# Performance work log

Measured on AMD Instinct MI355X. Metric: run time of the kernel, lower is better.

## Reference

```python
import jax, jax.numpy as jnp
import numpy as np

CONF_THR = 0.3   # cfg.THRESHOLD_PREDICT_CONF
NMS_THR = 0.5    # cfg.THRESHOLD_PREDICT_NMS
TOP_K = 2048     # fixed candidate budget (padded NMS, replaces boolean-mask gather)


def _build_grids():
    # YOLOv3 @ 608: feature maps 19/38/76, 3 anchors each -> HWA = 22743
    fsizes = [19, 38, 76]
    anchors_px = [
        [(116, 90), (156, 198), (373, 326)],
        [(30, 61), (62, 45), (59, 119)],
        [(10, 13), (16, 30), (33, 23)],
    ]
    img = 608.0
    gs, ans, ifs = [], [], []
    for fs, ancs in zip(fsizes, anchors_px):
        ys, xs = np.meshgrid(np.arange(fs), np.arange(fs), indexing='ij')
        cell = np.stack([xs, ys], -1).reshape(-1, 1, 2).astype(np.float32)
        cell = np.broadcast_to(cell, (fs * fs, 3, 2)).reshape(-1, 2)
        a = np.asarray(ancs, np.float32) / img
        a = np.broadcast_to(a[None], (fs * fs, 3, 2)).reshape(-1, 2)
        gs.append(cell)
        ans.append(np.ascontiguousarray(a))
        ifs.append(np.full((fs * fs * 3, 1), 1.0 / fs, np.float32))
    return (np.concatenate(gs), np.concatenate(ans), np.concatenate(ifs))


def setup_inputs() -> dict:
    key = jax.random.key(0)
    k1, k2, k3 = jax.random.split(key, 3)
    B, HWA, C = 32, 22743, 80
    grid_xy, anchor_wh, inv_fsize = _build_grids()
    return {
        'pconf': jax.random.normal(k1, (B, HWA, 1), jnp.float32),
        'pcls': jax.random.normal(k2, (B, HWA, C), jnp.float32),
        'ptxywh': jax.random.normal(k3, (B, HWA, 4), jnp.float32),
        'grid_xy': jnp.asarray(grid_xy),
        'anchor_wh': jnp.asarray(anchor_wh),
        'inv_fsize': jnp.asarray(inv_fsize),
    }


def _decode_ltrb(ptxywh, grid_xy, anchor_wh, inv_fsize):
    # boxes_decode4yolo3: cxcy = (sigmoid(txy)+grid)/fsize ; wh = exp(twh)*anchor
    cxcy = (jax.nn.sigmoid(ptxywh[..., :2]) + grid_xy) * inv_fsize
    wh = jnp.exp(ptxywh[..., 2:4]) * anchor_wh
    half = 0.5 * wh
    return jnp.concatenate([cxcy - half, cxcy + half], axis=-1)


def _iou_one_to_many(box, boxes):
    lt = jnp.maximum(box[:2], boxes[:, :2])
    rb = jnp.minimum(box[2:], boxes[:, 2:])
    wh = jnp.clip(rb - lt, 0.0)
    inter = wh[:, 0] * wh[:, 1]
    a1 = (box[2] - box[0]) * (box[3] - box[1])
    a2 = (boxes[:, 2] - boxes[:, 0]) * (boxes[:, 3] - boxes[:, 1])
    return inter / (a1 + a2 - inter + 1e-9)


def reference(pconf, pcls, ptxywh, grid_xy, anchor_wh, inv_fsize):
    B, HWA, C = pcls.shape
    conf = jax.nn.sigmoid(pconf[..., 0])                 # [B,HWA]
    cls_s = jax.nn.sigmoid(pcls)
    cls_conf = cls_s.max(-1)                             # [B,HWA]
    plabels = jnp.argmax(cls_s, -1).astype(jnp.int32) + 1  # labels +1 as original
    scores = cls_conf * conf                             # [B,HWA]
    pltrb = jnp.clip(_decode_ltrb(ptxywh, grid_xy, anchor_wh, inv_fsize), 0.0, 1.0)

    # threshold mask -> fixed top-K candidates (padded replacement for boolean gather)
    flat_scores = scores.reshape(-1)
    masked = jnp.where(flat_scores > CONF_THR, flat_scores, -1.0)
    top_s, top_i = jax.lax.top_k(masked, TOP_K)          # descending order
    valid = top_s > CONF_THR
    ids_b = (top_i // HWA).astype(jnp.int32)
    boxes = pltrb.reshape(-1, 4)[top_i]                  # [K,4]
    labels = plabels.reshape(-1)[top_i]                  # [K]
    scr = flat_scores[top_i]                             # [K]

    # per-(image,label) NMS via coordinate offset trick (label_nms equivalent)
    off = (ids_b.astype(jnp.float32) * (C + 2) + labels.astype(jnp.float32)) * 4.0
    boxes_off = boxes + off[:, None]
    idx = jnp.arange(TOP_K)

    def body(i, keep):
        iou = _iou_one_to_many(boxes_off[i], boxes_off)
        supp = keep[i] & (iou > NMS_THR) & (idx > i)
        return keep & ~supp

    keep = jax.lax.fori_loop(0, TOP_K, body, valid)
    scores_out = jnp.where(keep, scr, 0.0)
    boxes_out = jnp.where(keep[:, None], boxes, 0.0)
    return ids_b, boxes_out, labels, scores_out, keep
```

## Files before the change

### kernel.cpp

```cpp
#include <hip/hip_runtime.h>
#include <math.h>

#define HWA   22743
#define NBATCH 32
#define NROW  (HWA * NBATCH)
#define NC    80
#define TOPK  2048
#define CAND_CAP 4096
#define CONF_THR 0.3f
#define NMS_THR  0.5f
#define NBIN  4096
#define BIN0  0xBE999u
#define NZCAP 224

__device__ __forceinline__ unsigned int ford(float f) {
    unsigned int u = __float_as_uint(f);
    return (u & 0x80000000u) ? ~u : (u | 0x80000000u);
}
__device__ __forceinline__ float fdec(unsigned int o) {
    unsigned int u = (o & 0x80000000u) ? (o & 0x7fffffffu) : ~o;
    return __uint_as_float(u);
}
__device__ __forceinline__ float sigmoidf(float x) {
    return 1.0f / (1.0f + expf(-x));
}

__global__ void k_zero(unsigned int* __restrict__ z, int nwords) {
    int t = blockIdx.x * 1024 + threadIdx.x;
    if (t < nwords) z[t] = 0u;
}

__global__ void k_score(const float* __restrict__ pconf, const float* __restrict__ pcls,
                        unsigned int* __restrict__ skey, int* __restrict__ labels,
                        unsigned int* __restrict__ hist) {
    int gtid = blockIdx.x * blockDim.x + threadIdx.x;
    int wave = gtid >> 6;
    int lane = threadIdx.x & 63;
    int sub  = lane >> 4;
    int sl   = lane & 15;
    int nwaves = (gridDim.x * blockDim.x) >> 6;
    for (int base = wave * 4; base < NROW; base += nwaves * 4) {
        int i = base + sub;
        const float* row = pcls + (size_t)i * NC;
        float4 q = *(const float4*)(row + 4 * sl);
        float  e = row[64 + sl];
        float v0 = q.x; int i0 = 4 * sl;
        if (q.y > v0) { v0 = q.y; i0 = 4 * sl + 1; }
        if (q.z > v0) { v0 = q.z; i0 = 4 * sl + 2; }
        if (q.w > v0) { v0 = q.w; i0 = 4 * sl + 3; }
        if (e  > v0) { v0 = e;   i0 = 64 + sl; }
        #pragma unroll
        for (int off = 8; off > 0; off >>= 1) {
            float ov = __shfl_xor(v0, off, 64);
            int   oi = __shfl_xor(i0, off, 64);
            if (ov > v0 || (ov == v0 && oi < i0)) { v0 = ov; i0 = oi; }
        }
        if (sl == 0) {
            float cls_conf = sigmoidf(v0);
            float conf     = sigmoidf(pconf[i]);
            float score    = cls_conf * conf;
            float masked   = (score > CONF_THR) ? score : -1.0f;
            unsigned int o = ford(masked);
            skey[i]   = o;
            labels[i] = i0 + 1;
            if (score > CONF_THR) atomicAdd(&hist[(o >> 12) - BIN0], 1u);
        }
    }
}

__global__ __launch_bounds__(1024) void k_findT(const unsigned int* __restrict__ hist,
                                                unsigned int* __restrict__ scal) {
    __shared__ unsigned int a[1024];
    int tid = threadIdx.x;
    unsigned int r0 = hist[4095 - 4 * tid];
    unsigned int r1 = hist[4094 - 4 * tid];
    unsigned int r2 = hist[4093 - 4 * tid];
    unsigned int r3 = hist[4092 - 4 * tid];
    unsigned int local = r0 + r1 + r2 + r3;
    a[tid] = local;
    __syncthreads();
    for (int off = 1; off < 1024; off <<= 1) {
        unsigned int v = a[tid];
        unsigned int ad = (tid >= off) ? a[tid - off] : 0u;
        __syncthreads();
        a[tid] = v + ad;
        __syncthreads();
    }
    unsigned int inc = a[tid];
    unsigned int pre = inc - local;
    unsigned int total = a[1023];
    if (tid == 0 && total < TOPK) scal[0] = BIN0;
    if (pre < TOPK && inc >= TOPK) {
        unsigned int c = pre;
        unsigned int rr[4] = {r0, r1, r2, r3};
        #pragma unroll
        for (int j = 0; j < 4; ++j) {
            unsigned int nc = c + rr[j];
            if (c < TOPK && nc >= TOPK) {
                int p = 4 * tid + j;
                scal[0] = BIN0 + (unsigned int)(4095 - p);
            }
            c = nc;
        }
    }
}

__global__ void k_compact(const unsigned int* __restrict__ skey,
                          unsigned long long* __restrict__ cand,
                          unsigned int* __restrict__ scal) {
    unsigned int T = scal[0];
    int lane = threadIdx.x & 63;
    int stride = gridDim.x * blockDim.x;
    for (int i = blockIdx.x * blockDim.x + threadIdx.x; i < NROW; i += stride) {
        unsigned int o = skey[i];
        bool take = (o >> 12) >= T;
        unsigned long long m = __ballot(take);
        if (m) {
            int leader = __ffsll(m) - 1;
            unsigned int bse = 0;
            if (lane == leader) bse = atomicAdd(&scal[1], (unsigned int)__popcll(m));
            bse = __shfl(bse, leader, 64);
            if (take) {
                unsigned int pos = bse + (unsigned int)__popcll(m & ((1ull << lane) - 1ull));
                if (pos < CAND_CAP)
                    cand[pos] = ((unsigned long long)o << 32) | (unsigned int)(~(unsigned int)i);
            }
        }
    }
}

__global__ __launch_bounds__(256) void k_rank(const unsigned long long* __restrict__ cand,
                                              const unsigned int* __restrict__ scal,
                                              unsigned int* __restrict__ rankbuf) {
    __shared__ unsigned long long tile[256];
    unsigned int M = scal[1]; if (M > CAND_CAP) M = CAND_CAP;
    int ct = blockIdx.x >> 4;
    int st = blockIdx.x & 15;
    int c  = ct * 256 + threadIdx.x;
    int jb = st * 256;
    tile[threadIdx.x] = (jb + threadIdx.x < (int)M) ? cand[jb + threadIdx.x] : 0ull;
    __syncthreads();
    if (c < (int)M) {
        unsigned long long myk = cand[c];
        int lim = (int)M - jb; if (lim > 256) lim = 256;
        int r = 0;
        #pragma unroll 8
        for (int j = 0; j < lim; ++j) r += (tile[j] > myk) ? 1 : 0;
        if (r) atomicAdd(&rankbuf[c], (unsigned int)r);
    }
}

__global__ __launch_bounds__(256) void k_scatprep(const unsigned long long* __restrict__ cand,
                          const unsigned int* __restrict__ rankbuf,
                          const unsigned int* __restrict__ scal,
                          const int* __restrict__ labels,
                          const float* __restrict__ ptxywh,
                          const float* __restrict__ grid_xy,
                          const float* __restrict__ anchor_wh,
                          const float* __restrict__ inv_fsize,
                          unsigned int* __restrict__ bidx_a, unsigned int* __restrict__ label_a,
                          float* __restrict__ score_a, float4* __restrict__ box_a,
                          float4* __restrict__ boxoff_a, unsigned long long* __restrict__ keepmask) {
    unsigned int M = scal[1]; if (M > CAND_CAP) M = CAND_CAP;
    int t = blockIdx.x * 256 + threadIdx.x;
    if (t < (int)M) {
        unsigned int rk = rankbuf[t];
        if (rk < TOPK) {
            unsigned long long key = cand[t];
            unsigned int idx = ~(unsigned int)(key & 0xffffffffull);
            unsigned int o = (unsigned int)(key >> 32);
            float score = fdec(o);
            unsigned int b = idx / HWA;
            unsigned int r = idx - b * HWA;
            int lab = labels[idx];
            const float* tp = ptxywh + (size_t)idx * 4;
            float tx = tp[0], ty = tp[1], tw = tp[2], th = tp[3];
            float gx = grid_xy[2 * r], gy = grid_xy[2 * r + 1];
            float aw = anchor_wh[2 * r], ah = anchor_wh[2 * r + 1];
            float invf = inv_fsize[r];
            float cx = (sigmoidf(tx) + gx) * invf;
            float cy = (sigmoidf(ty) + gy) * invf;
            float w = expf(tw) * aw;
            float h = expf(th) * ah;
            float hx = 0.5f * w, hy = 0.5f * h;
            float l = cx - hx, tt = cy - hy, rr = cx + hx, bb = cy + hy;
            l  = fminf(fmaxf(l, 0.0f), 1.0f);
            tt = fminf(fmaxf(tt, 0.0f), 1.0f);
            rr = fminf(fmaxf(rr, 0.0f), 1.0f);
            bb = fminf(fmaxf(bb, 0.0f), 1.0f);
            float off = ((float)b * (float)(NC + 2) + (float)lab) * 4.0f;
            float4 bx; bx.x = l; bx.y = tt; bx.z = rr; bx.w = bb;
            float4 bo; bo.x = l + off; bo.y = tt + off; bo.z = rr + off; bo.w = bb + off;
            box_a[rk] = bx;
            boxoff_a[rk] = bo;
            bidx_a[rk] = b;
            label_a[rk] = (unsigned int)lab;
            score_a[rk] = score;
            atomicOr(&keepmask[rk >> 6], 1ull << (rk & 63));
        }
    } else if (t < TOPK) {
        float4 z; z.x = 0.0f; z.y = 0.0f; z.z = 0.0f; z.w = 0.0f;
        box_a[t] = z; boxoff_a[t] = z;
        bidx_a[t] = 0u; label_a[t] = 0u; score_a[t] = 0.0f;
    }
}

__global__ void k_supp(const float4* __restrict__ boxoff,
                       unsigned long long* __restrict__ supp,
                       unsigned long long* __restrict__ rownz) {
    __shared__ unsigned long long anyw;
    int i = blockIdx.x;
    if (threadIdx.x == 0) anyw = 0ull;
    __syncthreads();
    float4 bi = boxoff[i];
    float a1 = (bi.z - bi.x) * (bi.w - bi.y);
    unsigned long long myany = 0ull;
    for (int jt = 0; jt < 8; ++jt) {
        int j = jt * 256 + threadIdx.x;
        float4 bj = boxoff[j];
        float ltx = fmaxf(bi.x, bj.x), lty = fmaxf(bi.y, bj.y);
        float rbx = fminf(bi.z, bj.z), rby = fminf(bi.w, bj.w);
        float wx = rbx - ltx; if (wx < 0.0f) wx = 0.0f;
        float wy = rby - lty; if (wy < 0.0f) wy = 0.0f;
        float inter = wx * wy;
        float a2 = (bj.z - bj.x) * (bj.w - bj.y);
        float iou = inter / (a1 + a2 - inter + 1e-9f);
        unsigned long long m = __ballot(iou > NMS_THR);
        int w = jt * 4 + (threadIdx.x >> 6);
        if ((threadIdx.x & 63) == 0) supp[(size_t)i * 32 + w] = m;
        unsigned long long masked;
        int base = w * 64;
        if (base + 63 <= i) masked = 0ull;
        else if (base > i) masked = m;
        else {
            int d = i - base;
            unsigned long long le = (d == 63) ? ~0ull : ((1ull << (d + 1)) - 1ull);
            masked = m & ~le;
        }
        if ((threadIdx.x & 63) == 0) myany |= masked;
    }
    if ((threadIdx.x & 63) == 0 && myany) atomicOr(&anyw, myany);
    __syncthreads();
    if (threadIdx.x == 0 && anyw) atomicOr(&rownz[i >> 6], 1ull << (i & 63));
}

__global__ __launch_bounds__(256) void k_scanout(const unsigned long long* __restrict__ supp,
                        const unsigned long long* __restrict__ rownz,
                        const unsigned long long* __restrict__ keepmask,
                        const unsigned int* __restrict__ bidx_a,
                        const unsigned int* __restrict__ label_a,
                        const float* __restrict__ score_a,
                        const float4* __restrict__ box_a,
                        float* __restrict__ out) {
    __shared__ unsigned long long kw[32];
    __shared__ unsigned long long rz[32];
    __shared__ unsigned int base[33];
    __shared__ unsigned short rowid[NZCAP];
    __shared__ unsigned long long sm[NZCAP][32];
    int tid = threadIdx.x;
    if (tid < 32) { kw[tid] = keepmask[tid]; rz[tid] = rownz[tid]; }
    __syncthreads();
    if (tid == 0) {
        unsigned int acc = 0;
        for (int w = 0; w < 32; ++w) { base[w] = acc; acc += (unsigned int)__popcll(rz[w]); }
        base[32] = acc;
    }
    __syncthreads();
    unsigned int A = base[32];
    unsigned int Acap = (A < NZCAP) ? A : NZCAP;
    if (tid < 32) {
        unsigned long long m = rz[tid];
        unsigned int p = base[tid];
        while (m) {
            int b = __ffsll(m) - 1;
            if (p < NZCAP) rowid[p] = (unsigned short)(tid * 64 + b);
            ++p;
            m &= m - 1ull;
        }
    }
    __syncthreads();
    for (unsigned int p0 = 0; p0 < Acap; p0 += 8) {
        unsigned int p = p0 + (unsigned int)(tid >> 5);
        if (p < Acap) {
            int i = rowid[p];
            sm[p][tid & 31] = supp[(size_t)i * 32 + (tid & 31)];
        }
    }
    __syncthreads();
    for (int wi = 0; wi < 32; ++wi) {
        unsigned long long processed = 0ull;
        while (true) {
            unsigned long long act = kw[wi] & rz[wi] & ~processed;
            if (!act) break;
            int b = __ffsll(act) - 1;
            int i = wi * 64 + b;
            unsigned int p = base[wi] +
                (unsigned int)__popcll(rz[wi] & ((1ull << b) - 1ull));
            if (tid < 32) {
                unsigned long long rw = (p < NZCAP) ? sm[p][tid]
                                                    : supp[(size_t)i * 32 + tid];
                if (tid < wi) rw = 0ull;
                else if (tid == wi) {
                    unsigned long long le = (b == 63) ? ~0ull : ((1ull << (b + 1)) - 1ull);
                    rw &= ~le;
                }
                kw[tid] &= ~rw;
            }
            __syncthreads();
            processed |= (1ull << b);
        }
    }
    __syncthreads();
    for (int k = tid; k < TOPK; k += 256) {
        bool kp = (kw[k >> 6] >> (k & 63)) & 1ull;
        float4 bx = box_a[k];
        out[k] = (float)bidx_a[k];
        float* ob = out + TOPK + 4 * k;
        ob[0] = kp ? bx.x : 0.0f;
        ob[1] = kp ? bx.y : 0.0f;
        ob[2] = kp ? bx.z : 0.0f;
        ob[3] = kp ? bx.w : 0.0f;
        out[TOPK * 5 + k] = (float)label_a[k];
        out[TOPK * 6 + k] = kp ? score_a[k] : 0.0f;
        out[TOPK * 7 + k] = kp ? 1.0f : 0.0f;
    }
}

extern "C" void kernel_launch(void* const* d_in, const int* in_sizes, int n_in,
                              void* d_out, int out_size, void* d_ws, size_t ws_size,
                              hipStream_t stream) {
    const float* pconf     = (const float*)d_in[0];
    const float* pcls      = (const float*)d_in[1];
    const float* ptxywh    = (const float*)d_in[2];
    const float* grid_xy   = (const float*)d_in[3];
    const float* anchor_wh = (const float*)d_in[4];
    const float* inv_fsize = (const float*)d_in[5];
    float* out = (float*)d_out;

    char* ws = (char*)d_ws;
    const size_t O_HIST   = 0;
    const size_t O_SCAL   = O_HIST + NBIN * 4;
    const size_t O_ROWNZ  = O_SCAL + 64;
    const size_t O_KEEPM  = O_ROWNZ + 256;
    const size_t O_RANK   = O_KEEPM + 256;
    const size_t O_ZEND   = O_RANK + (size_t)CAND_CAP * 4;
    const int    ZERO_WORDS = (int)(O_ZEND / 4);
    const size_t O_CAND   = O_ZEND;
    const size_t O_SKEY   = O_CAND + (size_t)CAND_CAP * 8;
    const size_t O_LABELS = O_SKEY + (size_t)NROW * 4;
    const size_t O_BIDX   = O_LABELS + (size_t)NROW * 4;
    const size_t O_LAB2   = O_BIDX + (size_t)TOPK * 4;
    const size_t O_SCORE  = O_LAB2 + (size_t)TOPK * 4;
    const size_t O_BOX    = O_SCORE + (size_t)TOPK * 4;
    const size_t O_BOXOFF = O_BOX + (size_t)TOPK * 16;
    const size_t O_SUPP   = O_BOXOFF + (size_t)TOPK * 16;

    unsigned int* hist  = (unsigned int*)(ws + O_HIST);
    unsigned int* scal  = (unsigned int*)(ws + O_SCAL);
    unsigned long long* rownz = (unsigned long long*)(ws + O_ROWNZ);
    unsigned long long* keepm = (unsigned long long*)(ws + O_KEEPM);
    unsigned int* rankbuf = (unsigned int*)(ws + O_RANK);
    unsigned long long* cand   = (unsigned long long*)(ws + O_CAND);
    unsigned int* skey  = (unsigned int*)(ws + O_SKEY);
    int*          labels = (int*)(ws + O_LABELS);
    unsigned int* bidx_a  = (unsigned int*)(ws + O_BIDX);
    unsigned int* label_a = (unsigned int*)(ws + O_LAB2);
    float*        score_a = (float*)(ws + O_SCORE);
    float4*       box_a   = (float4*)(ws + O_BOX);
    float4*       boxoff_a = (float4*)(ws + O_BOXOFF);
    unsigned long long* supp = (unsigned long long*)(ws + O_SUPP);

    k_zero<<<9, 1024, 0, stream>>>((unsigned int*)ws, ZERO_WORDS);
    k_score<<<2048, 256, 0, stream>>>(pconf, pcls, skey, labels, hist);
    k_findT<<<1, 1024, 0, stream>>>(hist, scal);
    k_compact<<<1024, 256, 0, stream>>>(skey, cand, scal);
    k_rank<<<256, 256, 0, stream>>>(cand, scal, rankbuf);
    k_scatprep<<<CAND_CAP / 256, 256, 0, stream>>>(cand, rankbuf, scal, labels, ptxywh,
                                                   grid_xy, anchor_wh, inv_fsize,
                                                   bidx_a, label_a, score_a,
                                                   box_a, boxoff_a, keepm);
    k_supp<<<TOPK, 256, 0, stream>>>(boxoff_a, supp, rownz);
    k_scanout<<<1, 256, 0, stream>>>(supp, rownz, keepm, bidx_a, label_a, score_a,
                                     box_a, out);
}
```

Before: 168.4 us.

## Fuse post-score pipeline into one cooperative kernel with grid syncs

Replaces six separate launches (threshold search, compaction, ranking, scatter/decode, suppression matrix, scan/output) with a single cooperative kernel of 256 blocks. Grid-wide syncs separate the stages, and every block recomputes the threshold from the histogram itself. The suppression stage now stages all offset boxes in shared memory and each block handles 8 rows. This targets launch overhead and inter-kernel gaps in a latency-bound tail, at the cost of grid-sync overhead, reduced parallelism in the compaction and suppression stages, and a larger shared-memory footprint.

```diff
diff --git a/kernel.cpp b/kernel.cpp
--- a/kernel.cpp
+++ b/kernel.cpp
@@ -1,5 +1,8 @@
 #include <hip/hip_runtime.h>
+#include <hip/hip_cooperative_groups.h>
 #include <math.h>
+
+namespace cg = cooperative_groups;
 
 #define HWA   22743
 #define NBATCH 32
@@ -12,6 +15,23 @@
 #define NBIN  4096
 #define BIN0  0xBE999u
 #define NZCAP 224
+
+#define O_HIST   ((size_t)0)
+#define O_SCAL   (O_HIST + (size_t)NBIN * 4)
+#define O_ROWNZ  (O_SCAL + 64)
+#define O_KEEPM  (O_ROWNZ + 256)
+#define O_RANK   (O_KEEPM + 256)
+#define O_ZEND   (O_RANK + (size_t)CAND_CAP * 4)
+#define ZERO_WORDS ((int)(O_ZEND / 4))
+#define O_CAND   O_ZEND
+#define O_SKEY   (O_CAND + (size_t)CAND_CAP * 8)
+#define O_LABELS (O_SKEY + (size_t)NROW * 4)
+#define O_BIDX   (O_LABELS + (size_t)NROW * 4)
+#define O_LAB2   (O_BIDX + (size_t)TOPK * 4)
+#define O_SCORE  (O_LAB2 + (size_t)TOPK * 4)
+#define O_BOX    (O_SCORE + (size_t)TOPK * 4)
+#define O_BOXOFF (O_BOX + (size_t)TOPK * 16)
+#define O_SUPP   (O_BOXOFF + (size_t)TOPK * 16)
 
 __device__ __forceinline__ unsigned int ford(float f) {
     unsigned int u = __float_as_uint(f);
@@ -68,261 +88,273 @@
     }
 }
 
-__global__ __launch_bounds__(1024) void k_findT(const unsigned int* __restrict__ hist,
-                                                unsigned int* __restrict__ scal) {
-    __shared__ unsigned int a[1024];
+__global__ __launch_bounds__(256, 1) void k_tail(char* __restrict__ ws,
+        const float* __restrict__ ptxywh, const float* __restrict__ grid_xy,
+        const float* __restrict__ anchor_wh, const float* __restrict__ inv_fsize,
+        float* __restrict__ out) {
+    unsigned int* hist  = (unsigned int*)(ws + O_HIST);
+    unsigned int* scal  = (unsigned int*)(ws + O_SCAL);
+    unsigned long long* rownz = (unsigned long long*)(ws + O_ROWNZ);
+    unsigned long long* keepm = (unsigned long long*)(ws + O_KEEPM);
+    unsigned int* rankbuf = (unsigned int*)(ws + O_RANK);
+    unsigned long long* cand = (unsigned long long*)(ws + O_CAND);
+    unsigned int* skey  = (unsigned int*)(ws + O_SKEY);
+    const int* labels   = (const int*)(ws + O_LABELS);
+    unsigned int* bidx_a  = (unsigned int*)(ws + O_BIDX);
+    unsigned int* label_a = (unsigned int*)(ws + O_LAB2);
+    float*        score_a = (float*)(ws + O_SCORE);
+    float4*       box_a   = (float4*)(ws + O_BOX);
+    float4*       boxoff_a = (float4*)(ws + O_BOXOFF);
+    unsigned long long* supp = (unsigned long long*)(ws + O_SUPP);
+
+    cg::grid_group gg = cg::this_grid();
     int tid = threadIdx.x;
-    unsigned int r0 = hist[4095 - 4 * tid];
-    unsigned int r1 = hist[4094 - 4 * tid];
-    unsigned int r2 = hist[4093 - 4 * tid];
-    unsigned int r3 = hist[4092 - 4 * tid];
-    unsigned int local = r0 + r1 + r2 + r3;
-    a[tid] = local;
-    __syncthreads();
-    for (int off = 1; off < 1024; off <<= 1) {
-        unsigned int v = a[tid];
-        unsigned int ad = (tid >= off) ? a[tid - off] : 0u;
-        __syncthreads();
-        a[tid] = v + ad;
-        __syncthreads();
-    }
-    unsigned int inc = a[tid];
-    unsigned int pre = inc - local;
-    unsigned int total = a[1023];
-    if (tid == 0 && total < TOPK) scal[0] = BIN0;
-    if (pre < TOPK && inc >= TOPK) {
-        unsigned int c = pre;
-        unsigned int rr[4] = {r0, r1, r2, r3};
-        #pragma unroll
-        for (int j = 0; j < 4; ++j) {
-            unsigned int nc = c + rr[j];
-            if (c < TOPK && nc >= TOPK) {
-                int p = 4 * tid + j;
-                scal[0] = BIN0 + (unsigned int)(4095 - p);
-            }
-            c = nc;
-        }
-    }
-}
-
-__global__ void k_compact(const unsigned int* __restrict__ skey,
-                          unsigned long long* __restrict__ cand,
-                          unsigned int* __restrict__ scal) {
-    unsigned int T = scal[0];
-    int lane = threadIdx.x & 63;
-    int stride = gridDim.x * blockDim.x;
-    for (int i = blockIdx.x * blockDim.x + threadIdx.x; i < NROW; i += stride) {
-        unsigned int o = skey[i];
-        bool take = (o >> 12) >= T;
-        unsigned long long m = __ballot(take);
-        if (m) {
-            int leader = __ffsll(m) - 1;
-            unsigned int bse = 0;
-            if (lane == leader) bse = atomicAdd(&scal[1], (unsigned int)__popcll(m));
-            bse = __shfl(bse, leader, 64);
-            if (take) {
-                unsigned int pos = bse + (unsigned int)__popcll(m & ((1ull << lane) - 1ull));
-                if (pos < CAND_CAP)
-                    cand[pos] = ((unsigned long long)o << 32) | (unsigned int)(~(unsigned int)i);
-            }
-        }
-    }
-}
-
-__global__ __launch_bounds__(256) void k_rank(const unsigned long long* __restrict__ cand,
-                                              const unsigned int* __restrict__ scal,
-                                              unsigned int* __restrict__ rankbuf) {
-    __shared__ unsigned long long tile[256];
-    unsigned int M = scal[1]; if (M > CAND_CAP) M = CAND_CAP;
-    int ct = blockIdx.x >> 4;
-    int st = blockIdx.x & 15;
-    int c  = ct * 256 + threadIdx.x;
-    int jb = st * 256;
-    tile[threadIdx.x] = (jb + threadIdx.x < (int)M) ? cand[jb + threadIdx.x] : 0ull;
-    __syncthreads();
-    if (c < (int)M) {
-        unsigned long long myk = cand[c];
-        int lim = (int)M - jb; if (lim > 256) lim = 256;
-        int r = 0;
-        #pragma unroll 8
-        for (int j = 0; j < lim; ++j) r += (tile[j] > myk) ? 1 : 0;
-        if (r) atomicAdd(&rankbuf[c], (unsigned int)r);
-    }
-}
-
-__global__ __launch_bounds__(256) void k_scatprep(const unsigned long long* __restrict__ cand,
-                          const unsigned int* __restrict__ rankbuf,
-                          const unsigned int* __restrict__ scal,
-                          const int* __restrict__ labels,
-                          const float* __restrict__ ptxywh,
-                          const float* __restrict__ grid_xy,
-                          const float* __restrict__ anchor_wh,
-                          const float* __restrict__ inv_fsize,
-                          unsigned int* __restrict__ bidx_a, unsigned int* __restrict__ label_a,
-                          float* __restrict__ score_a, float4* __restrict__ box_a,
-                          float4* __restrict__ boxoff_a, unsigned long long* __restrict__ keepmask) {
-    unsigned int M = scal[1]; if (M > CAND_CAP) M = CAND_CAP;
-    int t = blockIdx.x * 256 + threadIdx.x;
-    if (t < (int)M) {
-        unsigned int rk = rankbuf[t];
-        if (rk < TOPK) {
-            unsigned long long key = cand[t];
-            unsigned int idx = ~(unsigned int)(key & 0xffffffffull);
-            unsigned int o = (unsigned int)(key >> 32);
-            float score = fdec(o);
-            unsigned int b = idx / HWA;
-            unsigned int r = idx - b * HWA;
-            int lab = labels[idx];
-            const float* tp = ptxywh + (size_t)idx * 4;
-            float tx = tp[0], ty = tp[1], tw = tp[2], th = tp[3];
-            float gx = grid_xy[2 * r], gy = grid_xy[2 * r + 1];
-            float aw = anchor_wh[2 * r], ah = anchor_wh[2 * r + 1];
-            float invf = inv_fsize[r];
-            float cx = (sigmoidf(tx) + gx) * invf;
-            float cy = (sigmoidf(ty) + gy) * invf;
-            float w = expf(tw) * aw;
-            float h = expf(th) * ah;
-            float hx = 0.5f * w, hy = 0.5f * h;
-            float l = cx - hx, tt = cy - hy, rr = cx + hx, bb = cy + hy;
-            l  = fminf(fmaxf(l, 0.0f), 1.0f);
-            tt = fminf(fmaxf(tt, 0.0f), 1.0f);
-            rr = fminf(fmaxf(rr, 0.0f), 1.0f);
-            bb = fminf(fmaxf(bb, 0.0f), 1.0f);
-            float off = ((float)b * (float)(NC + 2) + (float)lab) * 4.0f;
-            float4 bx; bx.x = l; bx.y = tt; bx.z = rr; bx.w = bb;
-            float4 bo; bo.x = l + off; bo.y = tt + off; bo.z = rr + off; bo.w = bb + off;
-            box_a[rk] = bx;
-            boxoff_a[rk] = bo;
-            bidx_a[rk] = b;
-            label_a[rk] = (unsigned int)lab;
-            score_a[rk] = score;
-            atomicOr(&keepmask[rk >> 6], 1ull << (rk & 63));
-        }
-    } else if (t < TOPK) {
-        float4 z; z.x = 0.0f; z.y = 0.0f; z.z = 0.0f; z.w = 0.0f;
-        box_a[t] = z; boxoff_a[t] = z;
-        bidx_a[t] = 0u; label_a[t] = 0u; score_a[t] = 0.0f;
-    }
-}
-
-__global__ void k_supp(const float4* __restrict__ boxoff,
-                       unsigned long long* __restrict__ supp,
-                       unsigned long long* __restrict__ rownz) {
-    __shared__ unsigned long long anyw;
-    int i = blockIdx.x;
-    if (threadIdx.x == 0) anyw = 0ull;
-    __syncthreads();
-    float4 bi = boxoff[i];
-    float a1 = (bi.z - bi.x) * (bi.w - bi.y);
-    unsigned long long myany = 0ull;
-    for (int jt = 0; jt < 8; ++jt) {
-        int j = jt * 256 + threadIdx.x;
-        float4 bj = boxoff[j];
-        float ltx = fmaxf(bi.x, bj.x), lty = fmaxf(bi.y, bj.y);
-        float rbx = fminf(bi.z, bj.z), rby = fminf(bi.w, bj.w);
-        float wx = rbx - ltx; if (wx < 0.0f) wx = 0.0f;
-        float wy = rby - lty; if (wy < 0.0f) wy = 0.0f;
-        float inter = wx * wy;
-        float a2 = (bj.z - bj.x) * (bj.w - bj.y);
-        float iou = inter / (a1 + a2 - inter + 1e-9f);
-        unsigned long long m = __ballot(iou > NMS_THR);
-        int w = jt * 4 + (threadIdx.x >> 6);
-        if ((threadIdx.x & 63) == 0) supp[(size_t)i * 32 + w] = m;
-        unsigned long long masked;
-        int base = w * 64;
-        if (base + 63 <= i) masked = 0ull;
-        else if (base > i) masked = m;
-        else {
-            int d = i - base;
-            unsigned long long le = (d == 63) ? ~0ull : ((1ull << (d + 1)) - 1ull);
-            masked = m & ~le;
-        }
-        if ((threadIdx.x & 63) == 0) myany |= masked;
-    }
-    if ((threadIdx.x & 63) == 0 && myany) atomicOr(&anyw, myany);
-    __syncthreads();
-    if (threadIdx.x == 0 && anyw) atomicOr(&rownz[i >> 6], 1ull << (i & 63));
-}
-
-__global__ __launch_bounds__(256) void k_scanout(const unsigned long long* __restrict__ supp,
-                        const unsigned long long* __restrict__ rownz,
-                        const unsigned long long* __restrict__ keepmask,
-                        const unsigned int* __restrict__ bidx_a,
-                        const unsigned int* __restrict__ label_a,
-                        const float* __restrict__ score_a,
-                        const float4* __restrict__ box_a,
-                        float* __restrict__ out) {
+    int bid = blockIdx.x;
+
+    __shared__ unsigned long long sm[NZCAP][32];
     __shared__ unsigned long long kw[32];
     __shared__ unsigned long long rz[32];
-    __shared__ unsigned int base[33];
+    __shared__ unsigned int sbase[33];
     __shared__ unsigned short rowid[NZCAP];
-    __shared__ unsigned long long sm[NZCAP][32];
-    int tid = threadIdx.x;
-    if (tid < 32) { kw[tid] = keepmask[tid]; rz[tid] = rownz[tid]; }
-    __syncthreads();
-    if (tid == 0) {
-        unsigned int acc = 0;
-        for (int w = 0; w < 32; ++w) { base[w] = acc; acc += (unsigned int)__popcll(rz[w]); }
-        base[32] = acc;
-    }
-    __syncthreads();
-    unsigned int A = base[32];
-    unsigned int Acap = (A < NZCAP) ? A : NZCAP;
-    if (tid < 32) {
-        unsigned long long m = rz[tid];
-        unsigned int p = base[tid];
-        while (m) {
-            int b = __ffsll(m) - 1;
-            if (p < NZCAP) rowid[p] = (unsigned short)(tid * 64 + b);
-            ++p;
-            m &= m - 1ull;
-        }
-    }
-    __syncthreads();
-    for (unsigned int p0 = 0; p0 < Acap; p0 += 8) {
-        unsigned int p = p0 + (unsigned int)(tid >> 5);
-        if (p < Acap) {
-            int i = rowid[p];
-            sm[p][tid & 31] = supp[(size_t)i * 32 + (tid & 31)];
-        }
-    }
-    __syncthreads();
-    for (int wi = 0; wi < 32; ++wi) {
-        unsigned long long processed = 0ull;
-        while (true) {
-            unsigned long long act = kw[wi] & rz[wi] & ~processed;
-            if (!act) break;
-            int b = __ffsll(act) - 1;
-            int i = wi * 64 + b;
-            unsigned int p = base[wi] +
-                (unsigned int)__popcll(rz[wi] & ((1ull << b) - 1ull));
-            if (tid < 32) {
-                unsigned long long rw = (p < NZCAP) ? sm[p][tid]
-                                                    : supp[(size_t)i * 32 + tid];
-                if (tid < wi) rw = 0ull;
-                else if (tid == wi) {
-                    unsigned long long le = (b == 63) ? ~0ull : ((1ull << (b + 1)) - 1ull);
-                    rw &= ~le;
+    __shared__ unsigned int sT;
+    __shared__ unsigned long long anyw;
+
+    {
+        unsigned int* a = (unsigned int*)sm;
+        unsigned int r[16];
+        unsigned int local = 0;
+        #pragma unroll
+        for (int j = 0; j < 16; ++j) {
+            r[j] = hist[4095 - (tid * 16 + j)];
+            local += r[j];
+        }
+        a[tid] = local;
+        __syncthreads();
+        for (int off = 1; off < 256; off <<= 1) {
+            unsigned int v = a[tid];
+            unsigned int ad = (tid >= off) ? a[tid - off] : 0u;
+            __syncthreads();
+            a[tid] = v + ad;
+            __syncthreads();
+        }
+        unsigned int inc = a[tid];
+        unsigned int pre = inc - local;
+        unsigned int total = a[255];
+        if (tid == 0 && total < TOPK) sT = BIN0;
+        if (pre < TOPK && inc >= TOPK) {
+            unsigned int c = pre;
+            #pragma unroll
+            for (int j = 0; j < 16; ++j) {
+                unsigned int nc = c + r[j];
+                if (c < TOPK && nc >= TOPK) {
+                    int p = tid * 16 + j;
+                    sT = BIN0 + (unsigned int)(4095 - p);
                 }
-                kw[tid] &= ~rw;
-            }
-            __syncthreads();
-            processed |= (1ull << b);
-        }
-    }
-    __syncthreads();
-    for (int k = tid; k < TOPK; k += 256) {
-        bool kp = (kw[k >> 6] >> (k & 63)) & 1ull;
-        float4 bx = box_a[k];
-        out[k] = (float)bidx_a[k];
-        float* ob = out + TOPK + 4 * k;
-        ob[0] = kp ? bx.x : 0.0f;
-        ob[1] = kp ? bx.y : 0.0f;
-        ob[2] = kp ? bx.z : 0.0f;
-        ob[3] = kp ? bx.w : 0.0f;
-        out[TOPK * 5 + k] = (float)label_a[k];
-        out[TOPK * 6 + k] = kp ? score_a[k] : 0.0f;
-        out[TOPK * 7 + k] = kp ? 1.0f : 0.0f;
+                c = nc;
+            }
+        }
+        __syncthreads();
+    }
+    unsigned int T = sT;
+
+    {
+        int lane = tid & 63;
+        int stride = 256 * 256;
+        for (int i = bid * 256 + tid; i < NROW; i += stride) {
+            unsigned int o = skey[i];
+            bool take = (o >> 12) >= T;
+            unsigned long long m = __ballot(take);
+            if (m) {
+                int leader = __ffsll(m) - 1;
+                unsigned int bse = 0;
+                if (lane == leader) bse = atomicAdd(&scal[1], (unsigned int)__popcll(m));
+                bse = __shfl(bse, leader, 64);
+                if (take) {
+                    unsigned int pos = bse + (unsigned int)__popcll(m & ((1ull << lane) - 1ull));
+                    if (pos < CAND_CAP)
+                        cand[pos] = ((unsigned long long)o << 32) | (unsigned int)(~(unsigned int)i);
+                }
+            }
+        }
+    }
+    gg.sync();
+
+    {
+        unsigned long long* tile = (unsigned long long*)sm;
+        unsigned int M = scal[1]; if (M > CAND_CAP) M = CAND_CAP;
+        int ct = bid >> 4;
+        int st = bid & 15;
+        int c  = ct * 256 + tid;
+        int jb = st * 256;
+        tile[tid] = (jb + tid < (int)M) ? cand[jb + tid] : 0ull;
+        __syncthreads();
+        if (c < (int)M) {
+            unsigned long long myk = cand[c];
+            int lim = (int)M - jb; if (lim > 256) lim = 256;
+            int r = 0;
+            #pragma unroll 8
+            for (int j = 0; j < lim; ++j) r += (tile[j] > myk) ? 1 : 0;
+            if (r) atomicAdd(&rankbuf[c], (unsigned int)r);
+        }
+    }
+    gg.sync();
+
+    if (bid < CAND_CAP / 256) {
+        unsigned int M = scal[1]; if (M > CAND_CAP) M = CAND_CAP;
+        int t = bid * 256 + tid;
+        if (t < (int)M) {
+            unsigned int rk = rankbuf[t];
+            if (rk < TOPK) {
+                unsigned long long key = cand[t];
+                unsigned int idx = ~(unsigned int)(key & 0xffffffffull);
+                unsigned int o = (unsigned int)(key >> 32);
+                float score = fdec(o);
+                unsigned int b = idx / HWA;
+                unsigned int r = idx - b * HWA;
+                int lab = labels[idx];
+                const float* tp = ptxywh + (size_t)idx * 4;
+                float tx = tp[0], ty = tp[1], tw = tp[2], th = tp[3];
+                float gx = grid_xy[2 * r], gy = grid_xy[2 * r + 1];
+                float aw = anchor_wh[2 * r], ah = anchor_wh[2 * r + 1];
+                float invf = inv_fsize[r];
+                float cx = (sigmoidf(tx) + gx) * invf;
+                float cy = (sigmoidf(ty) + gy) * invf;
+                float w = expf(tw) * aw;
+                float h = expf(th) * ah;
+                float hx = 0.5f * w, hy = 0.5f * h;
+                float l = cx - hx, tt = cy - hy, rr = cx + hx, bb = cy + hy;
+                l  = fminf(fmaxf(l, 0.0f), 1.0f);
+                tt = fminf(fmaxf(tt, 0.0f), 1.0f);
+                rr = fminf(fmaxf(rr, 0.0f), 1.0f);
+                bb = fminf(fmaxf(bb, 0.0f), 1.0f);
+                float off = ((float)b * (float)(NC + 2) + (float)lab) * 4.0f;
+                float4 bx; bx.x = l; bx.y = tt; bx.z = rr; bx.w = bb;
+                float4 bo; bo.x = l + off; bo.y = tt + off; bo.z = rr + off; bo.w = bb + off;
+                box_a[rk] = bx;
+                boxoff_a[rk] = bo;
+                bidx_a[rk] = b;
+                label_a[rk] = (unsigned int)lab;
+                score_a[rk] = score;
+                atomicOr(&keepm[rk >> 6], 1ull << (rk & 63));
+            }
+        } else if (t < TOPK) {
+            float4 z; z.x = 0.0f; z.y = 0.0f; z.z = 0.0f; z.w = 0.0f;
+            box_a[t] = z; boxoff_a[t] = z;
+            bidx_a[t] = 0u; label_a[t] = 0u; score_a[t] = 0.0f;
+        }
+    }
+    gg.sync();
+
+    {
+        float4* sbox = (float4*)sm;
+        for (int j = tid; j < TOPK; j += 256) sbox[j] = boxoff_a[j];
+        __syncthreads();
+        for (int r8 = 0; r8 < 8; ++r8) {
+            int i = bid * 8 + r8;
+            if (tid == 0) anyw = 0ull;
+            __syncthreads();
+            float4 bi = sbox[i];
+            float a1 = (bi.z - bi.x) * (bi.w - bi.y);
+            unsigned long long myany = 0ull;
+            for (int jt = 0; jt < 8; ++jt) {
+                int j = jt * 256 + tid;
+                float4 bj = sbox[j];
+                float ltx = fmaxf(bi.x, bj.x), lty = fmaxf(bi.y, bj.y);
+                float rbx = fminf(bi.z, bj.z), rby = fminf(bi.w, bj.w);
+                float wx = rbx - ltx; if (wx < 0.0f) wx = 0.0f;
+                float wy = rby - lty; if (wy < 0.0f) wy = 0.0f;
+                float inter = wx * wy;
+                float a2 = (bj.z - bj.x) * (bj.w - bj.y);
+                float iou = inter / (a1 + a2 - inter + 1e-9f);
+                unsigned long long m = __ballot(iou > NMS_THR);
+                int w = jt * 4 + (tid >> 6);
+                if ((tid & 63) == 0) supp[(size_t)i * 32 + w] = m;
+                unsigned long long masked;
+                int base = w * 64;
+                if (base + 63 <= i) masked = 0ull;
+                else if (base > i) masked = m;
+                else {
+                    int d = i - base;
+                    unsigned long long le = (d == 63) ? ~0ull : ((1ull << (d + 1)) - 1ull);
+                    masked = m & ~le;
+                }
+                if ((tid & 63) == 0) myany |= masked;
+            }
+            if ((tid & 63) == 0 && myany) atomicOr(&anyw, myany);
+            __syncthreads();
+            if (tid == 0 && anyw) atomicOr(&rownz[i >> 6], 1ull << (i & 63));
+            __syncthreads();
+        }
+    }
+    gg.sync();
+
+    if (bid == 0) {
+        if (tid < 32) { kw[tid] = keepm[tid]; rz[tid] = rownz[tid]; }
+        __syncthreads();
+        if (tid == 0) {
+            unsigned int acc = 0;
+            for (int w = 0; w < 32; ++w) { sbase[w] = acc; acc += (unsigned int)__popcll(rz[w]); }
+            sbase[32] = acc;
+        }
+        __syncthreads();
+        unsigned int A = sbase[32];
+        unsigned int Acap = (A < NZCAP) ? A : NZCAP;
+        if (tid < 32) {
+            unsigned long long m = rz[tid];
+            unsigned int p = sbase[tid];
+            while (m) {
+                int b = __ffsll(m) - 1;
+                if (p < NZCAP) rowid[p] = (unsigned short)(tid * 64 + b);
+                ++p;
+                m &= m - 1ull;
+            }
+        }
+        __syncthreads();
+        for (unsigned int p0 = 0; p0 < Acap; p0 += 8) {
+            unsigned int p = p0 + (unsigned int)(tid >> 5);
+            if (p < Acap) {
+                int i = rowid[p];
+                sm[p][tid & 31] = supp[(size_t)i * 32 + (tid & 31)];
+            }
+        }
+        __syncthreads();
+        for (int wi = 0; wi < 32; ++wi) {
+            unsigned long long processed = 0ull;
+            while (true) {
+                unsigned long long act = kw[wi] & rz[wi] & ~processed;
+                if (!act) break;
+                int b = __ffsll(act) - 1;
+                int i = wi * 64 + b;
+                unsigned int p = sbase[wi] +
+                    (unsigned int)__popcll(rz[wi] & ((1ull << b) - 1ull));
+                if (tid < 32) {
+                    unsigned long long rw = (p < NZCAP) ? sm[p][tid]
+                                                        : supp[(size_t)i * 32 + tid];
+                    if (tid < wi) rw = 0ull;
+                    else if (tid == wi) {
+                        unsigned long long le = (b == 63) ? ~0ull : ((1ull << (b + 1)) - 1ull);
+                        rw &= ~le;
+                    }
+                    kw[tid] &= ~rw;
+                }
+                __syncthreads();
+                processed |= (1ull << b);
+            }
+        }
+        __syncthreads();
+        for (int k = tid; k < TOPK; k += 256) {
+            bool kp = (kw[k >> 6] >> (k & 63)) & 1ull;
+            float4 bx = box_a[k];
+            out[k] = (float)bidx_a[k];
+            float* ob = out + TOPK + 4 * k;
+            ob[0] = kp ? bx.x : 0.0f;
+            ob[1] = kp ? bx.y : 0.0f;
+            ob[2] = kp ? bx.z : 0.0f;
+            ob[3] = kp ? bx.w : 0.0f;
+            out[TOPK * 5 + k] = (float)label_a[k];
+            out[TOPK * 6 + k] = kp ? score_a[k] : 0.0f;
+            out[TOPK * 7 + k] = kp ? 1.0f : 0.0f;
+        }
     }
 }
 
@@ -338,48 +370,14 @@
     float* out = (float*)d_out;
 
     char* ws = (char*)d_ws;
-    const size_t O_HIST   = 0;
-    const size_t O_SCAL   = O_HIST + NBIN * 4;
-    const size_t O_ROWNZ  = O_SCAL + 64;
-    const size_t O_KEEPM  = O_ROWNZ + 256;
-    const size_t O_RANK   = O_KEEPM + 256;
-    const size_t O_ZEND   = O_RANK + (size_t)CAND_CAP * 4;
-    const int    ZERO_WORDS = (int)(O_ZEND / 4);
-    const size_t O_CAND   = O_ZEND;
-    const size_t O_SKEY   = O_CAND + (size_t)CAND_CAP * 8;
-    const size_t O_LABELS = O_SKEY + (size_t)NROW * 4;
-    const size_t O_BIDX   = O_LABELS + (size_t)NROW * 4;
-    const size_t O_LAB2   = O_BIDX + (size_t)TOPK * 4;
-    const size_t O_SCORE  = O_LAB2 + (size_t)TOPK * 4;
-    const size_t O_BOX    = O_SCORE + (size_t)TOPK * 4;
-    const size_t O_BOXOFF = O_BOX + (size_t)TOPK * 16;
-    const size_t O_SUPP   = O_BOXOFF + (size_t)TOPK * 16;
-
-    unsigned int* hist  = (unsigned int*)(ws + O_HIST);
-    unsigned int* scal  = (unsigned int*)(ws + O_SCAL);
-    unsigned long long* rownz = (unsigned long long*)(ws + O_ROWNZ);
-    unsigned long long* keepm = (unsigned long long*)(ws + O_KEEPM);
-    unsigned int* rankbuf = (unsigned int*)(ws + O_RANK);
-    unsigned long long* cand   = (unsigned long long*)(ws + O_CAND);
     unsigned int* skey  = (unsigned int*)(ws + O_SKEY);
     int*          labels = (int*)(ws + O_LABELS);
-    unsigned int* bidx_a  = (unsigned int*)(ws + O_BIDX);
-    unsigned int* label_a = (unsigned int*)(ws + O_LAB2);
-    float*        score_a = (float*)(ws + O_SCORE);
-    float4*       box_a   = (float4*)(ws + O_BOX);
-    float4*       boxoff_a = (float4*)(ws + O_BOXOFF);
-    unsigned long long* supp = (unsigned long long*)(ws + O_SUPP);
+    unsigned int* hist  = (unsigned int*)(ws + O_HIST);
 
     k_zero<<<9, 1024, 0, stream>>>((unsigned int*)ws, ZERO_WORDS);
     k_score<<<2048, 256, 0, stream>>>(pconf, pcls, skey, labels, hist);
-    k_findT<<<1, 1024, 0, stream>>>(hist, scal);
-    k_compact<<<1024, 256, 0, stream>>>(skey, cand, scal);
-    k_rank<<<256, 256, 0, stream>>>(cand, scal, rankbuf);
-    k_scatprep<<<CAND_CAP / 256, 256, 0, stream>>>(cand, rankbuf, scal, labels, ptxywh,
-                                                   grid_xy, anchor_wh, inv_fsize,
-                                                   bidx_a, label_a, score_a,
-                                                   box_a, boxoff_a, keepm);
-    k_supp<<<TOPK, 256, 0, stream>>>(boxoff_a, supp, rownz);
-    k_scanout<<<1, 256, 0, stream>>>(supp, rownz, keepm, bidx_a, label_a, score_a,
-                                     box_a, out);
-}
+
+    void* args[] = {(void*)&ws, (void*)&ptxywh, (void*)&grid_xy,
+                    (void*)&anchor_wh, (void*)&inv_fsize, (void*)&out};
+    hipLaunchCooperativeKernel((void*)k_tail, dim3(256), dim3(256), args, 0, stream);
+}
```

Measured after the change: 284.5 us. +69.0%, slower.
